# Kernel optimization log

Hardware: AMD Instinct MI355X
Metric: run time of the kernel (lower is better)

## Reference

```python
import jax, jax.numpy as jnp
import numpy as np

N_QUBITS = 10
N_LAYERS = 3


def _apply_1q(state, gate, q, batched):
    # state: (B,) + (2,)*n ; gate: (2,2) or (B,2,2)
    s = jnp.moveaxis(state, q + 1, -1)
    shp = s.shape
    s = s.reshape(shp[0], -1, 2)
    eq = 'bij,brj->bri' if batched else 'ij,brj->bri'
    s = jnp.einsum(eq, gate, s).reshape(shp)
    return jnp.moveaxis(s, -1, q + 1)


def _apply_cnot(state, c, t):
    s = jnp.moveaxis(state, (c + 1, t + 1), (-2, -1))
    s = s.at[..., 1, :].set(s[..., 1, ::-1])  # flip target where control==1
    return jnp.moveaxis(s, (-2, -1), (c + 1, t + 1))


def _rot_gate(phi, theta, omega):
    # PennyLane Rot(phi,theta,omega) = RZ(omega) @ RY(theta) @ RZ(phi)
    ch = jnp.cos(theta * 0.5).astype(jnp.complex64)
    sh = jnp.sin(theta * 0.5).astype(jnp.complex64)
    m00 = jnp.exp(-1j * (phi + omega) * 0.5) * ch
    m01 = -jnp.exp(1j * (phi - omega) * 0.5) * sh
    m10 = jnp.exp(-1j * (phi - omega) * 0.5) * sh
    m11 = jnp.exp(1j * (phi + omega) * 0.5) * ch
    return jnp.stack([jnp.stack([m00, m01]), jnp.stack([m10, m11])])


def _circuit(x, weights):
    B = x.shape[0]
    n = N_QUBITS
    state = jnp.zeros((B,) + (2,) * n, jnp.complex64)
    state = state.at[(slice(None),) + (0,) * n].set(1.0)  # |0...0>
    c = jnp.cos(x * 0.5)  # (B, n)
    s = jnp.sin(x * 0.5)
    for l in range(N_LAYERS):
        # AngleEmbedding: RY(x_q) on each wire (batched gates)
        for q in range(n):
            g = jnp.stack([jnp.stack([c[:, q], -s[:, q]], -1),
                           jnp.stack([s[:, q], c[:, q]], -1)], -2).astype(jnp.complex64)
            state = _apply_1q(state, g, q, True)
        # StronglyEntanglingLayers, single sub-layer: Rot on each wire
        for q in range(n):
            g = _rot_gate(weights[l, q, 0], weights[l, q, 1], weights[l, q, 2])
            state = _apply_1q(state, g, q, False)
        # ring of CNOTs with range r=1
        for q in range(n):
            state = _apply_cnot(state, q, (q + 1) % n)
    probs = jnp.abs(state) ** 2  # (B,) + (2,)*n, real
    outs = []
    for q in range(n):
        axes = tuple(a for a in range(1, n + 1) if a != q + 1)
        m = probs.sum(axis=axes)  # (B, 2)
        outs.append(m[:, 0] - m[:, 1])  # <Z_q>
    return jnp.stack(outs, axis=1).astype(jnp.float32)


def setup_inputs() -> dict:
    key = jax.random.key(0)
    k1, k2 = jax.random.split(key)
    x = jax.random.normal(k1, (4096, N_QUBITS), dtype=jnp.float32)
    weights = jax.random.uniform(k2, (N_LAYERS, N_QUBITS, 3), dtype=jnp.float32,
                                 minval=-np.pi, maxval=np.pi)
    return {"x": x, "weights": weights}


def reference(x, weights):
    return _circuit(x, weights)
```

## Files before the change

kernel.cpp:

```cpp
#include <hip/hip_runtime.h>

#define NQ 10
#define NL 3

typedef float v2f __attribute__((ext_vector_type(2)));

__device__ __forceinline__ int   f2i(float v) { union { float f; int i; } u; u.f = v; return u.i; }
__device__ __forceinline__ float i2f(int v)   { union { int i; float f; } u; u.i = v; return u.f; }

__device__ __forceinline__ v2f cmul(v2f a, v2f b) {
    return (v2f){ fmaf(a.x, b.x, -a.y * b.y), fmaf(a.x, b.y, a.y * b.x) };
}

template<int C> __device__ __forceinline__ int dppm(int v) {
    return __builtin_amdgcn_mov_dpp(v, C, 0xF, 0xF, false);
}

template<int SP> __device__ __forceinline__ v2f pk_mul_sel(v2f a, v2f K) {
    v2f d;
    if constexpr (SP == 0)
        asm("v_pk_mul_f32 %0, %1, %2 op_sel:[0,0] op_sel_hi:[1,0]" : "=v"(d) : "v"(a), "v"(K));
    else
        asm("v_pk_mul_f32 %0, %1, %2 op_sel:[0,1] op_sel_hi:[1,1]" : "=v"(d) : "v"(a), "v"(K));
    return d;
}
template<int SP> __device__ __forceinline__ v2f pk_fma_sel(v2f a, v2f K, v2f c) {
    v2f d;
    if constexpr (SP == 0)
        asm("v_pk_fma_f32 %0, %1, %2, %3 op_sel:[0,0,0] op_sel_hi:[1,0,1]"
            : "=v"(d) : "v"(a), "v"(K), "v"(c));
    else
        asm("v_pk_fma_f32 %0, %1, %2, %3 op_sel:[0,1,0] op_sel_hi:[1,1,1]"
            : "=v"(d) : "v"(a), "v"(K), "v"(c));
    return d;
}
template<int SP> __device__ __forceinline__ v2f pk_fma_i_sel(v2f a, v2f K, v2f c) {
    v2f d;
    if constexpr (SP == 0)
        asm("v_pk_fma_f32 %0, %1, %2, %3 op_sel:[1,0,0] op_sel_hi:[0,0,1] neg_lo:[1,0,0]"
            : "=v"(d) : "v"(a), "v"(K), "v"(c));
    else
        asm("v_pk_fma_f32 %0, %1, %2, %3 op_sel:[1,1,0] op_sel_hi:[0,1,1] neg_lo:[1,0,0]"
            : "=v"(d) : "v"(a), "v"(K), "v"(c));
    return d;
}

template<int LM>
__device__ __forceinline__ v2f xlane(v2f v, int baddr) {
    if constexpr (LM == 0) return v;
    int x = f2i(v.x), y = f2i(v.y);
    if constexpr (LM == 1)       { x = dppm<177>(x);            y = dppm<177>(y); }
    else if constexpr (LM == 2)  { x = dppm<78>(x);             y = dppm<78>(y); }
    else if constexpr (LM == 3)  { x = dppm<27>(x);             y = dppm<27>(y); }
    else if constexpr (LM == 7)  { x = dppm<321>(x);            y = dppm<321>(y); }
    else if constexpr (LM == 15) { x = dppm<320>(x);            y = dppm<320>(y); }
    else if constexpr (LM == 4)  { x = dppm<321>(dppm<27>(x));  y = dppm<321>(dppm<27>(y)); }
    else if constexpr (LM == 5)  { x = dppm<321>(dppm<78>(x));  y = dppm<321>(dppm<78>(y)); }
    else if constexpr (LM == 6)  { x = dppm<321>(dppm<177>(x)); y = dppm<321>(dppm<177>(y)); }
    else if constexpr (LM == 8)  { x = dppm<320>(dppm<321>(x)); y = dppm<320>(dppm<321>(y)); }
    else if constexpr (LM == 12) { x = dppm<320>(dppm<27>(x));  y = dppm<320>(dppm<27>(y)); }
    else if constexpr (LM < 32) {
        constexpr int off = (LM << 10) | 0x1F;
        x = __builtin_amdgcn_ds_swizzle(x, off);
        y = __builtin_amdgcn_ds_swizzle(y, off);
    } else {
        x = __builtin_amdgcn_ds_bpermute(baddr, x);
        y = __builtin_amdgcn_ds_bpermute(baddr, y);
    }
    return (v2f){ i2f(x), i2f(y) };
}

template<int MASK, int RMASK>
__device__ __forceinline__ void apply_gate(v2f (&a)[16], float4 r0, float4 r1,
                                           float cq, float sq, int lane)
{
    constexpr int LM = (MASK >> 4) & 63;
    constexpr int JM = MASK & 15;
    constexpr int RH = (RMASK >> 4) & 63;
    constexpr int RL = RMASK & 15;

    const float g00r = fmaf(r0.x, cq,  r0.z * sq), g00i = fmaf(r0.y, cq,  r0.w * sq);
    const float g01r = fmaf(r0.z, cq, -r0.x * sq), g01i = fmaf(r0.w, cq, -r0.y * sq);
    const float g10r = fmaf(r1.x, cq,  r1.z * sq), g10i = fmaf(r1.y, cq,  r1.w * sq);
    const float g11r = fmaf(r1.z, cq, -r1.x * sq), g11i = fmaf(r1.w, cq, -r1.y * sq);

    const int lp = (RH != 0) ? (__popc(lane & RH) & 1) : 0;
    const v2f KAr = lp ? (v2f){g11r, g00r} : (v2f){g00r, g11r};
    const v2f KAi = lp ? (v2f){g11i, g00i} : (v2f){g00i, g11i};
    const v2f KBr = lp ? (v2f){g10r, g01r} : (v2f){g01r, g10r};
    const v2f KBi = lp ? (v2f){g10i, g01i} : (v2f){g01i, g10i};

    const int baddr = ((lane ^ LM) << 2);

    v2f o[16];
    #pragma unroll
    for (int j = 0; j < 16; ++j) o[j] = xlane<LM>(a[j ^ JM], baddr);

#define QNN_F(J) { constexpr int SP_ = __builtin_popcount((J) & RL) & 1;      \
    v2f t_ = pk_mul_sel<SP_>(a[J], KAr);                                      \
    t_ = pk_fma_i_sel<SP_>(a[J], KAi, t_);                                    \
    t_ = pk_fma_sel<SP_>(o[J], KBr, t_);                                      \
    t_ = pk_fma_i_sel<SP_>(o[J], KBi, t_);                                    \
    a[J] = t_; }
    QNN_F(0) QNN_F(1) QNN_F(2) QNN_F(3) QNN_F(4) QNN_F(5) QNN_F(6) QNN_F(7)
    QNN_F(8) QNN_F(9) QNN_F(10) QNN_F(11) QNN_F(12) QNN_F(13) QNN_F(14) QNN_F(15)
#undef QNN_F
}

__global__ __launch_bounds__(256, 4)
void qnn_kernel(const float* __restrict__ x, const float* __restrict__ w,
                float* __restrict__ out)
{
    __shared__ float4 rotL[NL * NQ][2];

    const int t    = threadIdx.x;
    const int lane = t & 63;
    const int b    = blockIdx.x * 4 + (t >> 6);

    if (t < NL * NQ) {
        const float* wp = w + t * 3;
        float phi = wp[0], th = wp[1], om = wp[2];
        float ct = cosf(th * 0.5f), st = sinf(th * 0.5f);
        float ap = (phi + om) * 0.5f, am = (phi - om) * 0.5f;
        float cap = cosf(ap), sap = sinf(ap);
        float cam = cosf(am), sam = sinf(am);
        rotL[t][0] = make_float4(cap * ct, -sap * ct, -cam * st, -sam * st);
        rotL[t][1] = make_float4(cam * st, -sam * st,  cap * ct,  sap * ct);
    }
    __syncthreads();

    const float* xb = x + (size_t)__builtin_amdgcn_readfirstlane(b * NQ);
    float c_[NQ], s_[NQ];
    #pragma unroll
    for (int q = 0; q < NQ; ++q) {
        float xv = xb[q] * 0.5f;
        c_[q] = i2f(__builtin_amdgcn_readfirstlane(f2i(__cosf(xv))));
        s_[q] = i2f(__builtin_amdgcn_readfirstlane(f2i(__sinf(xv))));
    }

    v2f c0[4], c1[4];
    v2f Ln = {1.f, 0.f};
    #pragma unroll
    for (int q = 0; q < NQ; ++q) {
        float4 r0 = rotL[q][0], r1 = rotL[q][1];
        float cq = c_[q], sq = s_[q];
        v2f g0 = { fmaf(r0.x, cq, r0.z * sq), fmaf(r0.y, cq, r0.w * sq) };
        v2f g1 = { fmaf(r1.x, cq, r1.z * sq), fmaf(r1.y, cq, r1.w * sq) };
        if (q < 4) { c0[q] = g0; c1[q] = g1; }
        else {
            v2f gg = ((lane >> (q - 4)) & 1) ? g1 : g0;
            Ln = (q == 4) ? gg : cmul(Ln, gg);
        }
    }
    v2f S01[4], SH[4];
    #pragma unroll
    for (int j = 0; j < 4; ++j)
        S01[j] = cmul((j & 1) ? c1[0] : c0[0], (j & 2) ? c1[1] : c0[1]);
    #pragma unroll
    for (int h = 0; h < 4; ++h)
        SH[h] = cmul(cmul((h & 1) ? c1[2] : c0[2], (h & 2) ? c1[3] : c0[3]), Ln);
    v2f a[16];
    #pragma unroll
    for (int j = 0; j < 16; ++j)
        a[j] = cmul(S01[j & 3], SH[j >> 2]);

#define GATE(IDX, Q, MASK, RMASK) \
    apply_gate<MASK, RMASK>(a, rotL[IDX][0], rotL[IDX][1], c_[Q], s_[Q], lane);
    GATE(10, 0, 0x003, 0x3FE)  GATE(11, 1, 0x006, 0x003)
    GATE(12, 2, 0x00C, 0x007)  GATE(13, 3, 0x018, 0x00F)
    GATE(14, 4, 0x030, 0x01F)  GATE(15, 5, 0x060, 0x03F)
    GATE(16, 6, 0x0C0, 0x07F)  GATE(17, 7, 0x180, 0x0FF)
    GATE(18, 8, 0x300, 0x1FF)  GATE(19, 9, 0x203, 0x3FF)
    GATE(20, 0, 0x005, 0x2AB)  GATE(21, 1, 0x00A, 0x3FD)
    GATE(22, 2, 0x014, 0x3FA)  GATE(23, 3, 0x028, 0x3F5)
    GATE(24, 4, 0x050, 0x3EA)  GATE(25, 5, 0x0A0, 0x3D5)
    GATE(26, 6, 0x140, 0x3AA)  GATE(27, 7, 0x280, 0x355)
    GATE(28, 8, 0x103, 0x2AA)  GATE(29, 9, 0x206, 0x155)
#undef GATE

    float P[16];
    #pragma unroll
    for (int j = 0; j < 16; ++j)
        P[j] = fmaf(a[j].x, a[j].x, a[j].y * a[j].y);
    #pragma unroll
    for (int bit = 0; bit < 4; ++bit) {
        #pragma unroll
        for (int j = 0; j < 16; ++j)
            if (!(j & (1 << bit))) {
                int k = j | (1 << bit);
                float u = P[j], v = P[k];
                P[j] = u + v;
                P[k] = u - v;
            }
    }

    const int bp32 = ((lane ^ 32) << 2);
    float vout = 0.f;
#define MEAS(Q, RM)                                                           \
    { constexpr int RH_ = ((RM) >> 4) & 63;                                   \
      constexpr int RL_ = (RM) & 15;                                          \
      float v = P[RL_];                                                       \
      if (__popc(lane & RH_) & 1) v = -v;                                     \
      v += i2f(dppm<177>(f2i(v)));                                 \
      v += i2f(dppm<78>(f2i(v)));                                  \
      v += i2f(dppm<321>(dppm<27>(f2i(v))));                  \
      v += i2f(dppm<320>(dppm<321>(f2i(v))));                \
      v += i2f(__builtin_amdgcn_ds_swizzle(f2i(v), (16 << 10) | 0x1F));       \
      v += i2f(__builtin_amdgcn_ds_bpermute(bp32, f2i(v)));                   \
      if (lane == (Q)) vout = v; }
    MEAS(0, 0x0CD) MEAS(1, 0x156) MEAS(2, 0x2AC) MEAS(3, 0x159)
    MEAS(4, 0x2B3) MEAS(5, 0x166) MEAS(6, 0x2CC) MEAS(7, 0x199)
    MEAS(8, 0x333) MEAS(9, 0x266)
#undef MEAS

    if (lane < NQ) out[b * NQ + lane] = vout;
}

extern "C" void kernel_launch(void* const* d_in, const int* in_sizes, int n_in,
                              void* d_out, int out_size, void* d_ws, size_t ws_size,
                              hipStream_t stream) {
    const float* x = (const float*)d_in[0];
    const float* w = (const float*)d_in[1];
    float* out = (float*)d_out;
    const int B = in_sizes[0] / NQ;
    qnn_kernel<<<B / 4, 256, 0, stream>>>(x, w, out);
}
```

Before: 78.42 us.

## Map two samples per wavefront with 32 amplitudes per lane

Changes the state-vector layout so each 64-lane wavefront simulates two batch samples, one per 32-lane half, with each lane holding 32 complex amplitudes instead of 16. More qubits become register-local, cross-lane traffic drops to DPP and swizzle with no bpermute, and the grid is halved. In exchange, per-lane register pressure roughly doubles, so launch bounds are lowered to 2 blocks per CU, which may reduce occupancy and latency hiding.

```diff
diff --git a/kernel.cpp b/kernel.cpp
--- a/kernel.cpp
+++ b/kernel.cpp
@@ -1,7 +1,6 @@
 #include <hip/hip_runtime.h>
 
 #define NQ 10
-#define NL 3
 
 typedef float v2f __attribute__((ext_vector_type(2)));
 
@@ -46,78 +45,102 @@
 }
 
 template<int LM>
-__device__ __forceinline__ v2f xlane(v2f v, int baddr) {
+__device__ __forceinline__ v2f xlane(v2f v) {
     if constexpr (LM == 0) return v;
     int x = f2i(v.x), y = f2i(v.y);
     if constexpr (LM == 1)       { x = dppm<177>(x);            y = dppm<177>(y); }
     else if constexpr (LM == 2)  { x = dppm<78>(x);             y = dppm<78>(y); }
     else if constexpr (LM == 3)  { x = dppm<27>(x);             y = dppm<27>(y); }
-    else if constexpr (LM == 7)  { x = dppm<321>(x);            y = dppm<321>(y); }
-    else if constexpr (LM == 15) { x = dppm<320>(x);            y = dppm<320>(y); }
-    else if constexpr (LM == 4)  { x = dppm<321>(dppm<27>(x));  y = dppm<321>(dppm<27>(y)); }
     else if constexpr (LM == 5)  { x = dppm<321>(dppm<78>(x));  y = dppm<321>(dppm<78>(y)); }
     else if constexpr (LM == 6)  { x = dppm<321>(dppm<177>(x)); y = dppm<321>(dppm<177>(y)); }
     else if constexpr (LM == 8)  { x = dppm<320>(dppm<321>(x)); y = dppm<320>(dppm<321>(y)); }
     else if constexpr (LM == 12) { x = dppm<320>(dppm<27>(x));  y = dppm<320>(dppm<27>(y)); }
-    else if constexpr (LM < 32) {
+    else {
         constexpr int off = (LM << 10) | 0x1F;
         x = __builtin_amdgcn_ds_swizzle(x, off);
         y = __builtin_amdgcn_ds_swizzle(y, off);
-    } else {
-        x = __builtin_amdgcn_ds_bpermute(baddr, x);
-        y = __builtin_amdgcn_ds_bpermute(baddr, y);
     }
     return (v2f){ i2f(x), i2f(y) };
 }
 
-template<int MASK, int RMASK>
-__device__ __forceinline__ void apply_gate(v2f (&a)[16], float4 r0, float4 r1,
-                                           float cq, float sq, int lane)
+struct Kset { v2f Ar, Ai, Br, Bi; };
+
+__device__ __forceinline__ Kset build_K(float4 r0, float4 r1, float cq, float sq, int lp)
 {
-    constexpr int LM = (MASK >> 4) & 63;
-    constexpr int JM = MASK & 15;
-    constexpr int RH = (RMASK >> 4) & 63;
-    constexpr int RL = RMASK & 15;
-
     const float g00r = fmaf(r0.x, cq,  r0.z * sq), g00i = fmaf(r0.y, cq,  r0.w * sq);
     const float g01r = fmaf(r0.z, cq, -r0.x * sq), g01i = fmaf(r0.w, cq, -r0.y * sq);
     const float g10r = fmaf(r1.x, cq,  r1.z * sq), g10i = fmaf(r1.y, cq,  r1.w * sq);
     const float g11r = fmaf(r1.z, cq, -r1.x * sq), g11i = fmaf(r1.w, cq, -r1.y * sq);
-
-    const int lp = (RH != 0) ? (__popc(lane & RH) & 1) : 0;
-    const v2f KAr = lp ? (v2f){g11r, g00r} : (v2f){g00r, g11r};
-    const v2f KAi = lp ? (v2f){g11i, g00i} : (v2f){g00i, g11i};
-    const v2f KBr = lp ? (v2f){g10r, g01r} : (v2f){g01r, g10r};
-    const v2f KBi = lp ? (v2f){g10i, g01i} : (v2f){g01i, g10i};
-
-    const int baddr = ((lane ^ LM) << 2);
-
-    v2f o[16];
-    #pragma unroll
-    for (int j = 0; j < 16; ++j) o[j] = xlane<LM>(a[j ^ JM], baddr);
-
-#define QNN_F(J) { constexpr int SP_ = __builtin_popcount((J) & RL) & 1;      \
-    v2f t_ = pk_mul_sel<SP_>(a[J], KAr);                                      \
-    t_ = pk_fma_i_sel<SP_>(a[J], KAi, t_);                                    \
-    t_ = pk_fma_sel<SP_>(o[J], KBr, t_);                                      \
-    t_ = pk_fma_i_sel<SP_>(o[J], KBi, t_);                                    \
-    a[J] = t_; }
-    QNN_F(0) QNN_F(1) QNN_F(2) QNN_F(3) QNN_F(4) QNN_F(5) QNN_F(6) QNN_F(7)
-    QNN_F(8) QNN_F(9) QNN_F(10) QNN_F(11) QNN_F(12) QNN_F(13) QNN_F(14) QNN_F(15)
+    Kset K;
+    K.Ar = lp ? (v2f){g11r, g00r} : (v2f){g00r, g11r};
+    K.Ai = lp ? (v2f){g11i, g00i} : (v2f){g00i, g11i};
+    K.Br = lp ? (v2f){g10r, g01r} : (v2f){g01r, g10r};
+    K.Bi = lp ? (v2f){g10i, g01i} : (v2f){g01i, g10i};
+    return K;
+}
+
+#define REP16(X, B) X(B) X(B|1) X(B|2) X(B|3) X(B|4) X(B|5) X(B|6) X(B|7) \
+                    X(B|8) X(B|9) X(B|10) X(B|11) X(B|12) X(B|13) X(B|14) X(B|15)
+
+template<int JM, int LM, int RJ, int RL>
+__device__ __forceinline__ void gate(v2f (&a)[32], float4 r0, float4 r1,
+                                     float cq, float sq, int lane)
+{
+    const int lp = (RL != 0) ? (__popc(lane & RL) & 1) : 0;
+    const Kset K = build_K(r0, r1, cq, sq, lp);
+#define QNN_F(J, O) { constexpr int SP_ = __builtin_popcount((J) & RJ) & 1;   \
+        v2f t_ = pk_mul_sel<SP_>(a[J], K.Ar);                                 \
+        t_ = pk_fma_i_sel<SP_>(a[J], K.Ai, t_);                               \
+        t_ = pk_fma_sel<SP_>(O, K.Br, t_);                                    \
+        t_ = pk_fma_i_sel<SP_>(O, K.Bi, t_);                                  \
+        a[J] = t_; }
+    if constexpr (JM < 16) {
+        {
+            v2f o[16];
+#define QNN_E(J) o[(J) & 15] = xlane<LM>(a[(J) ^ JM]);
+            REP16(QNN_E, 0)
+#undef QNN_E
+#define QNN_G(J) QNN_F(J, o[(J) & 15])
+            REP16(QNN_G, 0)
+#undef QNN_G
+        }
+        {
+            v2f o[16];
+#define QNN_E(J) o[(J) & 15] = xlane<LM>(a[(J) ^ JM]);
+            REP16(QNN_E, 16)
+#undef QNN_E
+#define QNN_G(J) QNN_F(J, o[(J) & 15])
+            REP16(QNN_G, 16)
+#undef QNN_G
+        }
+    } else {
+        constexpr int HB = 1 << (31 - __builtin_clz((unsigned)JM));
+#define QNN_P(J) if constexpr (((J) & HB) == 0) {                             \
+            constexpr int KP = (J) ^ JM;                                      \
+            v2f oj = xlane<LM>(a[KP]);                                        \
+            v2f ok = xlane<LM>(a[J]);                                         \
+            QNN_F(J, oj)                                                      \
+            QNN_F(KP, ok)                                                     \
+        }
+        REP16(QNN_P, 0)
+        REP16(QNN_P, 16)
+#undef QNN_P
+    }
 #undef QNN_F
 }
 
-__global__ __launch_bounds__(256, 4)
+__global__ __launch_bounds__(256, 2)
 void qnn_kernel(const float* __restrict__ x, const float* __restrict__ w,
                 float* __restrict__ out)
 {
-    __shared__ float4 rotL[NL * NQ][2];
+    __shared__ float4 rotL[3 * NQ][2];
 
     const int t    = threadIdx.x;
     const int lane = t & 63;
-    const int b    = blockIdx.x * 4 + (t >> 6);
-
-    if (t < NL * NQ) {
+    const int l5   = lane & 31;
+    const int b    = (blockIdx.x * 4 + (t >> 6)) * 2 + (lane >> 5);
+
+    if (t < 3 * NQ) {
         const float* wp = w + t * 3;
         float phi = wp[0], th = wp[1], om = wp[2];
         float ct = cosf(th * 0.5f), st = sinf(th * 0.5f);
@@ -129,63 +152,73 @@
     }
     __syncthreads();
 
-    const float* xb = x + (size_t)__builtin_amdgcn_readfirstlane(b * NQ);
+    const float* xb = x + (size_t)b * NQ;
     float c_[NQ], s_[NQ];
     #pragma unroll
     for (int q = 0; q < NQ; ++q) {
         float xv = xb[q] * 0.5f;
-        c_[q] = i2f(__builtin_amdgcn_readfirstlane(f2i(__cosf(xv))));
-        s_[q] = i2f(__builtin_amdgcn_readfirstlane(f2i(__sinf(xv))));
-    }
-
-    v2f c0[4], c1[4];
-    v2f Ln = {1.f, 0.f};
+        c_[q] = __cosf(xv);
+        s_[q] = __sinf(xv);
+    }
+
+    v2f a[32];
+    {
+        v2f g[NQ][2];
+        #pragma unroll
+        for (int q = 0; q < NQ; ++q) {
+            const float4 r0 = rotL[q][0], r1 = rotL[q][1];
+            g[q][0] = (v2f){ fmaf(r0.x, c_[q], r0.z * s_[q]),
+                             fmaf(r0.y, c_[q], r0.w * s_[q]) };
+            g[q][1] = (v2f){ fmaf(r1.x, c_[q], r1.z * s_[q]),
+                             fmaf(r1.y, c_[q], r1.w * s_[q]) };
+        }
+        const v2f F = cmul(cmul(cmul(g[5][l5 & 1], g[6][(l5 >> 1) & 1]),
+                                cmul(g[7][(l5 >> 2) & 1], g[8][(l5 >> 3) & 1])),
+                           g[9][(l5 >> 4) & 1]);
+        const v2f G4F[2] = { cmul(g[4][0], F), cmul(g[4][1], F) };
+        v2f S01[4], S23[4];
+        #pragma unroll
+        for (int i = 0; i < 4; ++i) {
+            S01[i] = cmul(g[0][i & 1], g[1][(i >> 1) & 1]);
+            S23[i] = cmul(g[2][i & 1], g[3][(i >> 1) & 1]);
+        }
+        #pragma unroll
+        for (int j = 0; j < 32; ++j)
+            a[j] = cmul(cmul(S01[j & 3], S23[(j >> 2) & 3]), G4F[(j >> 4) & 1]);
+    }
+
+#define G(IDX, Q, JM, LM, RJ, RL) \
+    gate<JM, LM, RJ, RL>(a, rotL[IDX][0], rotL[IDX][1], c_[Q], s_[Q], lane);
+    G(10, 0,  3,  0, 0x1E, 0x1F)
+    G(11, 1,  6,  0, 0x03, 0x00)
+    G(12, 2, 12,  0, 0x07, 0x00)
+    G(13, 3, 24,  0, 0x0F, 0x00)
+    G(14, 4, 16,  1, 0x1F, 0x00)
+    G(15, 5,  0,  3, 0x1F, 0x01)
+    G(16, 6,  0,  6, 0x1F, 0x03)
+    G(17, 7,  0, 12, 0x1F, 0x07)
+    G(18, 8,  0, 24, 0x1F, 0x0F)
+    G(19, 9,  3, 16, 0x1F, 0x1F)
+    G(20, 0,  5,  0,   11,   21)
+    G(21, 1, 10,  0,   29,   31)
+    G(22, 2, 20,  0,   26,   31)
+    G(23, 3,  8,  1,   21,   31)
+    G(24, 4, 16,  2,   10,   31)
+    G(25, 5,  0,  5,   21,   30)
+    G(26, 6,  0, 10,   10,   29)
+    G(27, 7,  0, 20,   21,   26)
+    G(28, 8,  3,  8,   10,   21)
+    G(29, 9,  6, 16,   21,   10)
+#undef G
+
+    float P[32];
     #pragma unroll
-    for (int q = 0; q < NQ; ++q) {
-        float4 r0 = rotL[q][0], r1 = rotL[q][1];
-        float cq = c_[q], sq = s_[q];
-        v2f g0 = { fmaf(r0.x, cq, r0.z * sq), fmaf(r0.y, cq, r0.w * sq) };
-        v2f g1 = { fmaf(r1.x, cq, r1.z * sq), fmaf(r1.y, cq, r1.w * sq) };
-        if (q < 4) { c0[q] = g0; c1[q] = g1; }
-        else {
-            v2f gg = ((lane >> (q - 4)) & 1) ? g1 : g0;
-            Ln = (q == 4) ? gg : cmul(Ln, gg);
-        }
-    }
-    v2f S01[4], SH[4];
-    #pragma unroll
-    for (int j = 0; j < 4; ++j)
-        S01[j] = cmul((j & 1) ? c1[0] : c0[0], (j & 2) ? c1[1] : c0[1]);
-    #pragma unroll
-    for (int h = 0; h < 4; ++h)
-        SH[h] = cmul(cmul((h & 1) ? c1[2] : c0[2], (h & 2) ? c1[3] : c0[3]), Ln);
-    v2f a[16];
-    #pragma unroll
-    for (int j = 0; j < 16; ++j)
-        a[j] = cmul(S01[j & 3], SH[j >> 2]);
-
-#define GATE(IDX, Q, MASK, RMASK) \
-    apply_gate<MASK, RMASK>(a, rotL[IDX][0], rotL[IDX][1], c_[Q], s_[Q], lane);
-    GATE(10, 0, 0x003, 0x3FE)  GATE(11, 1, 0x006, 0x003)
-    GATE(12, 2, 0x00C, 0x007)  GATE(13, 3, 0x018, 0x00F)
-    GATE(14, 4, 0x030, 0x01F)  GATE(15, 5, 0x060, 0x03F)
-    GATE(16, 6, 0x0C0, 0x07F)  GATE(17, 7, 0x180, 0x0FF)
-    GATE(18, 8, 0x300, 0x1FF)  GATE(19, 9, 0x203, 0x3FF)
-    GATE(20, 0, 0x005, 0x2AB)  GATE(21, 1, 0x00A, 0x3FD)
-    GATE(22, 2, 0x014, 0x3FA)  GATE(23, 3, 0x028, 0x3F5)
-    GATE(24, 4, 0x050, 0x3EA)  GATE(25, 5, 0x0A0, 0x3D5)
-    GATE(26, 6, 0x140, 0x3AA)  GATE(27, 7, 0x280, 0x355)
-    GATE(28, 8, 0x103, 0x2AA)  GATE(29, 9, 0x206, 0x155)
-#undef GATE
-
-    float P[16];
-    #pragma unroll
-    for (int j = 0; j < 16; ++j)
+    for (int j = 0; j < 32; ++j)
         P[j] = fmaf(a[j].x, a[j].x, a[j].y * a[j].y);
     #pragma unroll
-    for (int bit = 0; bit < 4; ++bit) {
-        #pragma unroll
-        for (int j = 0; j < 16; ++j)
+    for (int bit = 0; bit < 5; ++bit) {
+        #pragma unroll
+        for (int j = 0; j < 32; ++j)
             if (!(j & (1 << bit))) {
                 int k = j | (1 << bit);
                 float u = P[j], v = P[k];
@@ -194,26 +227,22 @@
             }
     }
 
-    const int bp32 = ((lane ^ 32) << 2);
     float vout = 0.f;
-#define MEAS(Q, RM)                                                           \
-    { constexpr int RH_ = ((RM) >> 4) & 63;                                   \
-      constexpr int RL_ = (RM) & 15;                                          \
-      float v = P[RL_];                                                       \
-      if (__popc(lane & RH_) & 1) v = -v;                                     \
+#define MEAS(Q, RJ_, RL_)                                                     \
+    { float v = P[RJ_];                                                       \
+      if (__popc(lane & (RL_)) & 1) v = -v;                                   \
       v += i2f(dppm<177>(f2i(v)));                                 \
       v += i2f(dppm<78>(f2i(v)));                                  \
-      v += i2f(dppm<321>(dppm<27>(f2i(v))));                  \
-      v += i2f(dppm<320>(dppm<321>(f2i(v))));                \
+      v += i2f(dppm<321>(dppm<27>(f2i(v))));                       \
+      v += i2f(dppm<320>(dppm<321>(f2i(v))));                      \
       v += i2f(__builtin_amdgcn_ds_swizzle(f2i(v), (16 << 10) | 0x1F));       \
-      v += i2f(__builtin_amdgcn_ds_bpermute(bp32, f2i(v)));                   \
-      if (lane == (Q)) vout = v; }
-    MEAS(0, 0x0CD) MEAS(1, 0x156) MEAS(2, 0x2AC) MEAS(3, 0x159)
-    MEAS(4, 0x2B3) MEAS(5, 0x166) MEAS(6, 0x2CC) MEAS(7, 0x199)
-    MEAS(8, 0x333) MEAS(9, 0x266)
+      if (l5 == (Q)) vout = v; }
+    MEAS(0, 13,  6) MEAS(1, 22, 10) MEAS(2, 12, 21) MEAS(3, 25, 10)
+    MEAS(4, 19, 21) MEAS(5,  6, 11) MEAS(6, 12, 22) MEAS(7, 25, 12)
+    MEAS(8, 19, 25) MEAS(9,  6, 19)
 #undef MEAS
 
-    if (lane < NQ) out[b * NQ + lane] = vout;
+    if (l5 < NQ) out[(size_t)b * NQ + l5] = vout;
 }
 
 extern "C" void kernel_launch(void* const* d_in, const int* in_sizes, int n_in,
@@ -223,5 +252,5 @@
     const float* w = (const float*)d_in[1];
     float* out = (float*)d_out;
     const int B = in_sizes[0] / NQ;
-    qnn_kernel<<<B / 4, 256, 0, stream>>>(x, w, out);
-}
+    qnn_kernel<<<B / 8, 256, 0, stream>>>(x, w, out);
+}
```

Measured after the change: 78.60 us. No clear change (+0.2%).
